# Kernel tuning notes

Hardware: AMD Instinct MI355X
Metric: run time of the kernel (lower is better)

Reference implementation:

```python
import jax, jax.numpy as jnp
import numpy as np
from jax import lax

N = 32768      # total nodes (8 graphs x 4096)
E = 262144     # edges (avg degree 8)
B = 8          # graphs in batch
TW = 25        # time window
H = 128        # hidden features
L = 6          # GNN layers
NV = 1         # n_variables (pos_t only)
SD = 1         # spatial dim
TMAX, TMIN, RES_T = 4.0, 0.0, 250.0
BD_LOW, BD_UP = 0.0, 16.0
EPS = 1e-5


def swish(x):
    return x * jax.nn.sigmoid(x)


def setup_inputs() -> dict:
    key = jax.random.key(0)
    ks = jax.random.split(key, 32)
    s = 0.05
    u = jax.random.normal(ks[0], (N, TW), jnp.float32)
    pos_t = jax.random.uniform(ks[1], (N, 1), jnp.float32) * TMAX
    pos_x = jax.random.uniform(ks[2], (N, 1), jnp.float32) * BD_UP
    pos = jnp.concatenate([pos_t, pos_x], axis=-1)
    edge_index = jax.random.randint(ks[3], (2, E), 0, N, jnp.int64)
    batch = jnp.repeat(jnp.arange(B, dtype=jnp.int64), N // B)
    d_in = TW + SD + NV          # 27
    d_msg = 2 * H + TW + SD + NV  # 282
    d_upd = H + H + NV            # 257
    We1 = jax.random.normal(ks[4], (d_in, H), jnp.float32) * s
    be1 = jnp.zeros((H,), jnp.float32)
    We2 = jax.random.normal(ks[5], (H, H), jnp.float32) * s
    be2 = jnp.zeros((H,), jnp.float32)
    Wm1 = jax.random.normal(ks[6], (L, d_msg, H), jnp.float32) * s
    bm1 = jnp.zeros((L, H), jnp.float32)
    Wm2 = jax.random.normal(ks[7], (L, H, H), jnp.float32) * s
    bm2 = jnp.zeros((L, H), jnp.float32)
    Wu1 = jax.random.normal(ks[8], (L, d_upd, H), jnp.float32) * s
    bu1 = jnp.zeros((L, H), jnp.float32)
    Wu2 = jax.random.normal(ks[9], (L, H, H), jnp.float32) * s
    bu2 = jnp.zeros((L, H), jnp.float32)
    Wc1 = jax.random.normal(ks[10], (8, 1, 16), jnp.float32) * s  # OIH
    bc1 = jnp.zeros((8,), jnp.float32)
    Wc2 = jax.random.normal(ks[11], (1, 8, 14), jnp.float32) * s
    bc2 = jnp.zeros((1,), jnp.float32)
    return dict(u=u, pos=pos, edge_index=edge_index, batch=batch,
                We1=We1, be1=be1, We2=We2, be2=be2,
                Wm1=Wm1, bm1=bm1, Wm2=Wm2, bm2=bm2,
                Wu1=Wu1, bu1=bu1, Wu2=Wu2, bu2=bu2,
                Wc1=Wc1, bc1=bc1, Wc2=Wc2, bc2=bc2)


def _mpnn(u, pos, edge_index, batch, We1, be1, We2, be2,
          Wm1, bm1, Wm2, bm2, Wu1, bu1, Wu2, bu2, Wc1, bc1, Wc2, bc2):
    src = edge_index[0]   # j (source)
    tgt = edge_index[1]   # i (target)
    pos_t = pos[:, 0:1] / TMAX
    pos_x = (pos[:, 1:] - BD_LOW) / (BD_UP - BD_LOW)
    variables = pos_t  # eq_variables empty -> only normalized time

    node_input = jnp.concatenate([u, pos_x, variables], axis=-1)  # [N, 27]
    h = swish(node_input @ We1 + be1)
    h = swish(h @ We2 + be2)

    # in-degree for scatter-mean (empty targets -> 0 like PyG mean)
    cnt = jnp.zeros((N,), jnp.float32).at[tgt].add(1.0)
    cnt = jnp.maximum(cnt, 1.0)[:, None]
    # per-graph node counts for InstanceNorm
    gcnt = jax.ops.segment_sum(jnp.ones((N,), jnp.float32), batch, num_segments=B)[:, None]

    u_diff_e = u[tgt] - u[src]          # [E, TW]
    p_diff_e = pos_x[tgt] - pos_x[src]  # [E, SD]
    var_i_e = variables[tgt]            # [E, NV]

    for l in range(L):
        # message: gather -> MLP per edge
        m_in = jnp.concatenate([h[tgt], h[src], u_diff_e, p_diff_e, var_i_e], axis=-1)  # [E, 282]
        msg = swish(m_in @ Wm1[l] + bm1[l])
        msg = swish(msg @ Wm2[l] + bm2[l])
        # scatter-mean aggregate onto targets
        agg = jax.ops.segment_sum(msg, tgt, num_segments=N) / cnt  # [N, H]
        # node update MLP, residual (in_features == out_features)
        up = jnp.concatenate([h, agg, variables], axis=-1)  # [N, 257]
        up = swish(up @ Wu1[l] + bu1[l])
        up = swish(up @ Wu2[l] + bu2[l])
        h = h + up
        # InstanceNorm per graph (no affine), biased variance
        mean = jax.ops.segment_sum(h, batch, num_segments=B) / gcnt      # [B, H]
        sq = jax.ops.segment_sum(h * h, batch, num_segments=B) / gcnt    # [B, H]
        var = sq - mean * mean
        h = (h - mean[batch]) / jnp.sqrt(var[batch] + EPS)

    # output CNN: tw=25 branch
    hc = h[:, None, :]  # [N, 1, 128]
    dn = ('NCH', 'OIH', 'NCH')
    c = lax.conv_general_dilated(hc, Wc1, (3,), 'VALID', dimension_numbers=dn) + bc1[None, :, None]
    c = swish(c)
    c = lax.conv_general_dilated(c, Wc2, (1,), 'VALID', dimension_numbers=dn) + bc2[None, :, None]
    diff = c[:, 0, :]  # [N, 25]

    dt = (TMAX - TMIN) / RES_T
    dt_cum = jnp.arange(1, TW + 1, dtype=jnp.float32) * dt  # cumsum of ones*dt
    out = u[:, -1:] + dt_cum[None, :] * diff
    return out


def reference(u, pos, edge_index, batch, We1, be1, We2, be2,
              Wm1, bm1, Wm2, bm2, Wu1, bu1, Wu2, bu2, Wc1, bc1, Wc2, bc2):
    return _mpnn(u, pos, edge_index, batch, We1, be1, We2, be2,
                 Wm1, bm1, Wm2, bm2, Wu1, bu1, Wu2, bu2, Wc1, bc1, Wc2, bc2)
```

## Files before the change

### kernel.cpp

```cpp
#include <hip/hip_runtime.h>
#include <stdint.h>

#define N_NODES 32768
#define N_EDGES 262144
#define NB 8
#define TW 25

typedef __attribute__((ext_vector_type(8))) short short8;
typedef __attribute__((ext_vector_type(4))) float floatx4;

#if defined(__has_builtin)
#if __has_builtin(__builtin_amdgcn_cvt_pk_bf16_f32)
#define HAVE_CVT_PK_BF16 1
#endif
#endif

__device__ __forceinline__ float swishf(float x) {
    return x * __builtin_amdgcn_rcpf(1.0f + __expf(-x));
}

__device__ __forceinline__ unsigned short f2bf(float x) {
    union { float f; unsigned u; } v; v.f = x;
    unsigned r = v.u + 0x7FFFu + ((v.u >> 16) & 1u);
    return (unsigned short)(r >> 16);
}
__device__ __forceinline__ unsigned pkbf(float a, float b) {
#ifdef HAVE_CVT_PK_BF16
    typedef __attribute__((ext_vector_type(2))) __bf16 bf16x2;
    union { bf16x2 v; unsigned u; } cv;
    cv.v = __builtin_amdgcn_cvt_pk_bf16_f32(a, b);
    return cv.u;
#else
    return (unsigned)f2bf(a) | ((unsigned)f2bf(b) << 16);
#endif
}
__device__ __forceinline__ float bf2f(unsigned short b) {
    union { unsigned u; float f; } v; v.u = ((unsigned)b) << 16; return v.f;
}
__device__ __forceinline__ float bflo(unsigned w) {
    union { unsigned u; float f; } v; v.u = w << 16; return v.f;
}
__device__ __forceinline__ float bfhi(unsigned w) {
    union { unsigned u; float f; } v; v.u = w & 0xffff0000u; return v.f;
}

__global__ void init_kernel(const float* __restrict__ pos, const float* __restrict__ u,
                            float* __restrict__ posx, float* __restrict__ post,
                            unsigned short* __restrict__ feat) {
    int i = blockIdx.x * 256 + threadIdx.x;
    if (i < N_NODES) {
        float pt = pos[i * 2 + 0] * 0.25f;
        float px = pos[i * 2 + 1] * 0.0625f;
        post[i] = pt;
        posx[i] = px;
        unsigned short f[32];
        #pragma unroll
        for (int k = 0; k < 25; ++k) f[k] = f2bf(u[(size_t)i * 25 + k]);
        f[25] = f2bf(px);
        f[26] = f2bf(pt);
        #pragma unroll
        for (int k = 27; k < 32; ++k) f[k] = 0;
        #pragma unroll
        for (int j = 0; j < 4; ++j)
            *(uint4*)(feat + (size_t)i * 32 + j * 8) = *(uint4*)&f[j * 8];
    }
}

__global__ void deg_kernel(const int* __restrict__ tgt, int* __restrict__ deg) {
    int i = blockIdx.x * 256 + threadIdx.x;
    if (i < N_EDGES) atomicAdd(&deg[tgt[i]], 1);
}

__global__ __launch_bounds__(1024) void scan_kernel(const int* __restrict__ deg,
                                                    int* __restrict__ cursor) {
    __shared__ int ps[1024];
    int t = threadIdx.x;
    int base = t * 32;
    int tot = 0;
    for (int i = 0; i < 32; ++i) tot += deg[base + i];
    ps[t] = tot;
    __syncthreads();
    for (int off = 1; off < 1024; off <<= 1) {
        int v = (t >= off) ? ps[t - off] : 0;
        __syncthreads();
        ps[t] += v;
        __syncthreads();
    }
    int run = ps[t] - tot;
    for (int i = 0; i < 32; ++i) {
        cursor[base + i] = run;
        run += deg[base + i];
    }
}

__global__ void scatter_kernel(const int* __restrict__ src, const int* __restrict__ tgt,
                               int* __restrict__ cursor,
                               int* __restrict__ src_s, int* __restrict__ tgt_s) {
    int i = blockIdx.x * 256 + threadIdx.x;
    if (i < N_EDGES) {
        int tg = tgt[i];
        int p = atomicAdd(&cursor[tg], 1);
        src_s[p] = src[i];
        tgt_s[p] = tg;
    }
}

__global__ __launch_bounds__(256) void pack_kernel(const float* __restrict__ W,
                                                   unsigned short* __restrict__ Wp,
                                                   int Kreal, int Kc, int total) {
    int id = blockIdx.x * 256 + threadIdx.x;
    if (id >= total) return;
    int lane = id & 63;
    int t8 = (id >> 6) & 7;
    int rest = id >> 9;
    int c = rest % Kc;
    int l = rest / Kc;
    int n = t8 * 16 + (lane & 15);
    int kb = c * 32 + (lane >> 4) * 8;
    short8 v;
    #pragma unroll
    for (int j = 0; j < 8; ++j) {
        int k = kb + j;
        float x = (k < Kreal) ? W[((size_t)l * Kreal + k) * 128 + n] : 0.f;
        v[j] = (short)f2bf(x);
    }
    *(short8*)(Wp + (size_t)id * 8) = v;
}

__global__ __launch_bounds__(256) void pack_cat_kernel(const float* __restrict__ Wm1,
                                                       const float* __restrict__ Wu1,
                                                       unsigned short* __restrict__ Wp) {
    int id = blockIdx.x * 256 + threadIdx.x;
    if (id >= 46080) return;
    int lane = id & 63;
    int tmp = id >> 6;
    int tile = tmp % 24;
    int tmp2 = tmp / 24;
    int c = tmp2 % 5;
    int l = tmp2 / 5;
    int n = tile * 16 + (lane & 15);
    int grp = n >> 7;
    int col = n & 127;
    int kb = c * 32 + (lane >> 4) * 8;
    const float* Wm = Wm1 + (size_t)l * 283 * 128;
    const float* Wu = Wu1 + (size_t)l * 257 * 128;
    short8 v;
    #pragma unroll
    for (int j = 0; j < 8; ++j) {
        int k = kb + j;
        float x = 0.f;
        if (grp == 2) {
            if (k < 128) x = Wu[(size_t)k * 128 + col];
        } else if (k < 128) {
            x = Wm[(size_t)(grp ? 128 + k : k) * 128 + col];
        } else if (k < 155) {
            int row = 256 + (k - 128);
            x = Wm[(size_t)row * 128 + col];
            if (grp) x = (row == 282) ? 0.f : -x;
        }
        v[j] = (short)f2bf(x);
    }
    *(short8*)(Wp + (size_t)id * 8) = v;
}

__global__ __launch_bounds__(256) void pack_upd_kernel(const float* __restrict__ Wu1,
                                                       unsigned short* __restrict__ Wp) {
    int id = blockIdx.x * 256 + threadIdx.x;
    if (id >= 15360) return;
    int lane = id & 63;
    int t8 = (id >> 6) & 7;
    int rest = id >> 9;
    int c = rest % 5;
    int l = rest / 5;
    int n = t8 * 16 + (lane & 15);
    int kb = c * 32 + (lane >> 4) * 8;
    const float* Wu = Wu1 + (size_t)l * 257 * 128;
    short8 v;
    #pragma unroll
    for (int j = 0; j < 8; ++j) {
        int k = kb + j;
        float x = 0.f;
        if (k < 128) x = Wu[(size_t)(128 + k) * 128 + n];
        else if (k == 128) x = Wu[(size_t)256 * 128 + n];
        v[j] = (short)f2bf(x);
    }
    *(short8*)(Wp + (size_t)id * 8) = v;
}

__global__ __launch_bounds__(256) void encoder_kernel(
    const float* __restrict__ u, const float* __restrict__ posx,
    const float* __restrict__ post,
    const float* __restrict__ We1, const float* __restrict__ be1,
    const float* __restrict__ We2, const float* __restrict__ be2,
    unsigned short* __restrict__ hraw, float* __restrict__ agg)
{
    __shared__ __align__(16) float As_[64 * 36];
    __shared__ __align__(16) float Ws[32 * 128];
    __shared__ __align__(16) float Ms[64 * 128];

    int t = threadIdx.x;
    int n0 = blockIdx.x * 64;
    int rg = t >> 5, cg = t & 31;

    {
        int r = t & 63, cseg = t >> 6;
        float4 z = make_float4(0.f, 0.f, 0.f, 0.f);
        #pragma unroll
        for (int j = 0; j < 8; ++j)
            *(float4*)(agg + (size_t)(n0 + r) * 128 + cseg * 32 + j * 4) = z;
    }

    float acc[8][4] = {};
    {
        int kk = t >> 3, cb = (t & 7) * 16;
        #pragma unroll
        for (int j = 0; j < 4; ++j) {
            float4 w = make_float4(0.f, 0.f, 0.f, 0.f);
            if (kk < 27) w = *(const float4*)&We1[kk * 128 + cb + j * 4];
            *(float4*)&Ws[kk * 128 + cb + j * 4] = w;
        }
        int el = t >> 2, kb = (t & 3) * 8, n = n0 + el;
        float v[8];
        #pragma unroll
        for (int j = 0; j < 8; ++j) {
            int k = kb + j;
            float x = 0.f;
            if (k < 25) x = u[n * 25 + k];
            else if (k == 25) x = posx[n];
            else if (k == 26) x = post[n];
            v[j] = x;
        }
        #pragma unroll
        for (int j = 0; j < 8; j += 4)
            *(float4*)&As_[el * 36 + kb + j] = make_float4(v[j], v[j+1], v[j+2], v[j+3]);
        __syncthreads();
        #pragma unroll 4
        for (int kk2 = 0; kk2 < 32; ++kk2) {
            float4 b = *(const float4*)&Ws[kk2 * 128 + cg * 4];
            float a[8];
            #pragma unroll
            for (int i = 0; i < 8; ++i) a[i] = As_[(rg * 8 + i) * 36 + kk2];
            #pragma unroll
            for (int i = 0; i < 8; ++i) {
                acc[i][0] += a[i] * b.x; acc[i][1] += a[i] * b.y;
                acc[i][2] += a[i] * b.z; acc[i][3] += a[i] * b.w;
            }
        }
        __syncthreads();
    }
    {
        float4 b1 = *(const float4*)&be1[cg * 4];
        #pragma unroll
        for (int i = 0; i < 8; ++i) {
            float4 m;
            m.x = swishf(acc[i][0] + b1.x);
            m.y = swishf(acc[i][1] + b1.y);
            m.z = swishf(acc[i][2] + b1.z);
            m.w = swishf(acc[i][3] + b1.w);
            *(float4*)&Ms[(rg * 8 + i) * 128 + cg * 4] = m;
        }
        __syncthreads();
    }
    float acc2[8][4] = {};
    for (int k0 = 0; k0 < 128; k0 += 32) {
        int kk = t >> 3, cb = (t & 7) * 16;
        #pragma unroll
        for (int j = 0; j < 4; ++j)
            *(float4*)&Ws[kk * 128 + cb + j * 4] =
                *(const float4*)&We2[(k0 + kk) * 128 + cb + j * 4];
        __syncthreads();
        #pragma unroll 4
        for (int kk2 = 0; kk2 < 32; ++kk2) {
            float4 b = *(const float4*)&Ws[kk2 * 128 + cg * 4];
            float a[8];
            #pragma unroll
            for (int i = 0; i < 8; ++i) a[i] = Ms[(rg * 8 + i) * 128 + (k0 + kk2)];
            #pragma unroll
            for (int i = 0; i < 8; ++i) {
                acc2[i][0] += a[i] * b.x; acc2[i][1] += a[i] * b.y;
                acc2[i][2] += a[i] * b.z; acc2[i][3] += a[i] * b.w;
            }
        }
        __syncthreads();
    }
    {
        float4 b2 = *(const float4*)&be2[cg * 4];
        #pragma unroll
        for (int i = 0; i < 8; ++i) {
            int n = n0 + rg * 8 + i;
            float4 o;
            o.x = swishf(acc2[i][0] + b2.x);
            o.y = swishf(acc2[i][1] + b2.y);
            o.z = swishf(acc2[i][2] + b2.z);
            o.w = swishf(acc2[i][3] + b2.w);
            uint2 pk;
            pk.x = pkbf(o.x, o.y);
            pk.y = pkbf(o.z, o.w);
            *(uint2*)(hraw + (size_t)n * 128 + cg * 4) = pk;
        }
    }
}

__global__ __launch_bounds__(512, 4) void premsg_kernel(
    const unsigned short* __restrict__ hraw,
    const float* __restrict__ stats_prev, int donorm,
    const unsigned short* __restrict__ feat,
    const unsigned short* __restrict__ Wp,
    const float* __restrict__ b1, const float* __restrict__ bu1,
    unsigned short* __restrict__ At, unsigned short* __restrict__ As,
    unsigned short* __restrict__ Uh)
{
    __shared__ __align__(16) unsigned short A[64 * 168];
    __shared__ float mean_s[128];
    __shared__ float rstd_s[128];

    int t = threadIdx.x;
    int n0 = blockIdx.x * 64;
    int bidx = n0 >> 12;

    if (t < 128) {
        float mn = 0.f, rs = 1.f;
        if (donorm) {
            float s1 = stats_prev[bidx * 128 + t] * (1.f / 4096.f);
            float s2 = stats_prev[(NB + bidx) * 128 + t] * (1.f / 4096.f);
            mn = s1;
            rs = rsqrtf(s2 - s1 * s1 + 1e-5f);
        }
        mean_s[t] = mn;
        rstd_s[t] = rs;
    }
    __syncthreads();

    {
        int r = t & 63, cseg = t >> 6;
        int n = n0 + r;
        uint4 raw0 = *(const uint4*)(hraw + (size_t)n * 128 + cseg * 16);
        uint4 raw1 = *(const uint4*)(hraw + (size_t)n * 128 + cseg * 16 + 8);
        unsigned pk[8];
        #pragma unroll
        for (int j = 0; j < 8; ++j) {
            unsigned word = (j < 4) ? ((const unsigned*)&raw0)[j]
                                    : ((const unsigned*)&raw1)[j - 4];
            int c0 = cseg * 16 + j * 2;
            float v0 = (bf2f((unsigned short)(word & 0xffffu)) - mean_s[c0]) * rstd_s[c0];
            float v1 = (bf2f((unsigned short)(word >> 16)) - mean_s[c0 + 1]) * rstd_s[c0 + 1];
            pk[j] = pkbf(v0, v1);
        }
        *(uint4*)(A + r * 168 + cseg * 16)     = *(uint4*)&pk[0];
        *(uint4*)(A + r * 168 + cseg * 16 + 8) = *(uint4*)&pk[4];
        if (cseg < 2) {
            uint4 f0 = *(const uint4*)(feat + (size_t)n * 32 + cseg * 16);
            uint4 f1 = *(const uint4*)(feat + (size_t)n * 32 + cseg * 16 + 8);
            *(uint4*)(A + r * 168 + 128 + cseg * 16)     = f0;
            *(uint4*)(A + r * 168 + 128 + cseg * 16 + 8) = f1;
        }
    }
    __syncthreads();

    int w = t >> 6, lane = t & 63, q = lane >> 4, m = lane & 15;
    floatx4 accT[4] = {};
    floatx4 accS[4] = {};
    floatx4 accU[4] = {};
    #pragma unroll
    for (int c = 0; c < 5; ++c) {
        short8 bT = *(const short8*)(Wp + ((size_t)(c * 24 + w) * 64 + lane) * 8);
        short8 bS = *(const short8*)(Wp + ((size_t)(c * 24 + 8 + w) * 64 + lane) * 8);
        short8 bU = *(const short8*)(Wp + ((size_t)(c * 24 + 16 + w) * 64 + lane) * 8);
        #pragma unroll
        for (int g2 = 0; g2 < 4; ++g2) {
            short8 a = *(const short8*)(A + (g2 * 16 + m) * 168 + c * 32 + q * 8);
            accT[g2] = __builtin_amdgcn_mfma_f32_16x16x32_bf16(a, bT, accT[g2], 0, 0, 0);
            accS[g2] = __builtin_amdgcn_mfma_f32_16x16x32_bf16(a, bS, accS[g2], 0, 0, 0);
            accU[g2] = __builtin_amdgcn_mfma_f32_16x16x32_bf16(a, bU, accU[g2], 0, 0, 0);
        }
    }
    int col = w * 16 + m;
    float bvT = b1[col];
    float bvU = bu1[col];
    #pragma unroll
    for (int g2 = 0; g2 < 4; ++g2) {
        #pragma unroll
        for (int r = 0; r < 4; ++r) {
            int row = g2 * 16 + q * 4 + r;
            size_t idx = (size_t)(n0 + row) * 128 + col;
            At[idx] = f2bf(accT[g2][r] + bvT);
            As[idx] = f2bf(accS[g2][r]);
        }
    }
    {
        unsigned up[8];
        #pragma unroll
        for (int g2 = 0; g2 < 4; ++g2) {
            up[g2 * 2]     = pkbf(accU[g2][0] + bvU, accU[g2][1] + bvU);
            up[g2 * 2 + 1] = pkbf(accU[g2][2] + bvU, accU[g2][3] + bvU);
        }
        unsigned short* dst = Uh + (size_t)blockIdx.x * 8192 + t * 16;
        *(uint4*)dst       = *(uint4*)&up[0];
        *(uint4*)(dst + 8) = *(uint4*)&up[4];
    }
}

__global__ __launch_bounds__(256, 8) void message_kernel(
    const unsigned short* __restrict__ At, const unsigned short* __restrict__ As,
    const int* __restrict__ src_s, const int* __restrict__ tgt_s,
    const unsigned short* __restrict__ W2p, const float* __restrict__ b2,
    float* __restrict__ agg, float* __restrict__ stats_cur)
{
    __shared__ __align__(16) unsigned short Cs[64 * 132];
    __shared__ int tgtS[64];

    int t = threadIdx.x;
    int e0 = blockIdx.x * 64;
    if (blockIdx.x == 0) {
        float4 z = make_float4(0.f, 0.f, 0.f, 0.f);
        *(float4*)&stats_cur[t * 8] = z;
        *(float4*)&stats_cur[t * 8 + 4] = z;
    }
    if (t < 64) tgtS[t] = tgt_s[e0 + t];
    __syncthreads();

    int w = t >> 6, lane = t & 63, q = lane >> 4, m = lane & 15;
    int erow = w * 16 + m;
    int e = e0 + erow;
    int gg = tgtS[erow];
    int ss = src_s[e];

    const unsigned short* atp = At + (size_t)gg * 128 + q * 8;
    const unsigned short* asp = As + (size_t)ss * 128 + q * 8;
    uint4 wa[4], wb[4];
    #pragma unroll
    for (int c = 0; c < 4; ++c) {
        wa[c] = *(const uint4*)(atp + c * 32);
        wb[c] = *(const uint4*)(asp + c * 32);
    }
    short8 af[4];
    #pragma unroll
    for (int c = 0; c < 4; ++c) {
        const unsigned* ua = (const unsigned*)&wa[c];
        const unsigned* ub = (const unsigned*)&wb[c];
        union { unsigned u[4]; short8 s; } pk_;
        #pragma unroll
        for (int j = 0; j < 4; ++j) {
            float lo = swishf(bflo(ua[j]) + bflo(ub[j]));
            float hi = swishf(bfhi(ua[j]) + bfhi(ub[j]));
            pk_.u[j] = pkbf(lo, hi);
        }
        af[c] = pk_.s;
    }

    floatx4 acc[8] = {};
    #pragma unroll
    for (int c = 0; c < 4; ++c) {
        #pragma unroll
        for (int t8 = 0; t8 < 8; ++t8) {
            short8 b = *(const short8*)(W2p + ((size_t)(c * 8 + t8) * 64 + lane) * 8);
            acc[t8] = __builtin_amdgcn_mfma_f32_16x16x32_bf16(af[c], b, acc[t8], 0, 0, 0);
        }
    }

    #pragma unroll
    for (int t8 = 0; t8 < 8; ++t8) {
        float bv = b2[t8 * 16 + m];
        unsigned p01 = pkbf(swishf(acc[t8][0] + bv), swishf(acc[t8][1] + bv));
        unsigned p23 = pkbf(swishf(acc[t8][2] + bv), swishf(acc[t8][3] + bv));
        int rb = (w * 16 + q * 4) * 132 + t8 * 16 + m;
        Cs[rb]           = (unsigned short)p01;
        Cs[rb + 132]     = (unsigned short)(p01 >> 16);
        Cs[rb + 2 * 132] = (unsigned short)p23;
        Cs[rb + 3 * 132] = (unsigned short)(p23 >> 16);
    }

    {
        int r0 = w * 16;
        int col0 = lane;
        float run0 = 0.f, run1 = 0.f;
        int prev = tgtS[r0];
        bool atStart = true;
        #pragma unroll 4
        for (int i = 0; i < 16; ++i) {
            int tg = tgtS[r0 + i];
            if (tg != prev) {
                float* d0 = &agg[(size_t)prev * 128 + col0];
                if (atStart) { atomicAdd(d0, run0); atomicAdd(d0 + 64, run1); }
                else         { d0[0] = run0;        d0[64] = run1; }
                run0 = 0.f; run1 = 0.f; prev = tg; atStart = false;
            }
            run0 += bf2f(Cs[(r0 + i) * 132 + col0]);
            run1 += bf2f(Cs[(r0 + i) * 132 + col0 + 64]);
        }
        float* d0 = &agg[(size_t)prev * 128 + col0];
        atomicAdd(d0, run0);
        atomicAdd(d0 + 64, run1);
    }
}

__global__ __launch_bounds__(512, 8) void update_kernel(
    unsigned short* __restrict__ hraw,
    const unsigned short* __restrict__ Uh,
    float* __restrict__ agg, const int* __restrict__ deg,
    const float* __restrict__ post,
    const float* __restrict__ stats_prev, int donorm,
    const unsigned short* __restrict__ W1p,
    const unsigned short* __restrict__ W2p, const float* __restrict__ b2,
    float* __restrict__ stats_cur)
{
    __shared__ __align__(16) unsigned short A[64 * 168];
    __shared__ __align__(16) unsigned short Msh[64 * 136];

    int t = threadIdx.x;
    int n0 = blockIdx.x * 64;
    int bidx = n0 >> 12;

    const unsigned short* usrc = Uh + (size_t)blockIdx.x * 8192 + t * 16;
    uint4 uh0 = *(const uint4*)usrc;
    uint4 uh1 = *(const uint4*)(usrc + 8);

    {
        int r = t & 63, cseg = t >> 6;
        int n = n0 + r;
        float ic = __builtin_amdgcn_rcpf(fmaxf((float)deg[n], 1.0f));
        const float* ap = agg + (size_t)n * 128 + cseg * 16;
        float4 v0 = *(const float4*)ap;
        float4 v1 = *(const float4*)(ap + 4);
        float4 v2 = *(const float4*)(ap + 8);
        float4 v3 = *(const float4*)(ap + 12);
        unsigned pa[8];
        pa[0] = pkbf(v0.x * ic, v0.y * ic);
        pa[1] = pkbf(v0.z * ic, v0.w * ic);
        pa[2] = pkbf(v1.x * ic, v1.y * ic);
        pa[3] = pkbf(v1.z * ic, v1.w * ic);
        pa[4] = pkbf(v2.x * ic, v2.y * ic);
        pa[5] = pkbf(v2.z * ic, v2.w * ic);
        pa[6] = pkbf(v3.x * ic, v3.y * ic);
        pa[7] = pkbf(v3.z * ic, v3.w * ic);
        *(uint4*)(A + r * 168 + cseg * 16)     = *(uint4*)&pa[0];
        *(uint4*)(A + r * 168 + cseg * 16 + 8) = *(uint4*)&pa[4];
        if (cseg < 4) {
            short8 z;
            #pragma unroll
            for (int k = 0; k < 8; ++k) z[k] = 0;
            if (cseg == 0) z[0] = (short)f2bf(post[n]);
            *(short8*)(A + r * 168 + 128 + cseg * 8) = z;
        }
    }
    __syncthreads();

    int w = t >> 6, lane = t & 63, q = lane >> 4, m = lane & 15;
    int col = w * 16 + m;

    floatx4 acc[4] = {};
    #pragma unroll
    for (int c = 0; c < 5; ++c) {
        short8 b = *(const short8*)(W1p + ((size_t)(c * 8 + w) * 64 + lane) * 8);
        #pragma unroll
        for (int g2 = 0; g2 < 4; ++g2) {
            short8 a = *(const short8*)(A + (g2 * 16 + m) * 168 + c * 32 + q * 8);
            acc[g2] = __builtin_amdgcn_mfma_f32_16x16x32_bf16(a, b, acc[g2], 0, 0, 0);
        }
    }
    {
        const unsigned* uu0 = (const unsigned*)&uh0;
        const unsigned* uu1 = (const unsigned*)&uh1;
        #pragma unroll
        for (int g2 = 0; g2 < 4; ++g2) {
            unsigned wlo = (g2 < 2) ? uu0[g2 * 2]     : uu1[(g2 - 2) * 2];
            unsigned whi = (g2 < 2) ? uu0[g2 * 2 + 1] : uu1[(g2 - 2) * 2 + 1];
            int rowb = g2 * 16 + q * 4;
            float v0 = swishf(acc[g2][0] + bflo(wlo));
            float v1 = swishf(acc[g2][1] + bfhi(wlo));
            float v2 = swishf(acc[g2][2] + bflo(whi));
            float v3 = swishf(acc[g2][3] + bfhi(whi));
            unsigned p01 = pkbf(v0, v1);
            unsigned p23 = pkbf(v2, v3);
            Msh[(rowb + 0) * 136 + col] = (unsigned short)p01;
            Msh[(rowb + 1) * 136 + col] = (unsigned short)(p01 >> 16);
            Msh[(rowb + 2) * 136 + col] = (unsigned short)p23;
            Msh[(rowb + 3) * 136 + col] = (unsigned short)(p23 >> 16);
        }
    }
    __syncthreads();

    floatx4 acc2[4] = {};
    #pragma unroll
    for (int c = 0; c < 4; ++c) {
        short8 b = *(const short8*)(W2p + ((size_t)(c * 8 + w) * 64 + lane) * 8);
        #pragma unroll
        for (int g2 = 0; g2 < 4; ++g2) {
            short8 a = *(const short8*)(Msh + (g2 * 16 + m) * 136 + c * 32 + q * 8);
            acc2[g2] = __builtin_amdgcn_mfma_f32_16x16x32_bf16(a, b, acc2[g2], 0, 0, 0);
        }
    }

    float mn = 0.f, rs = 1.f;
    if (donorm) {
        float s1 = stats_prev[bidx * 128 + col] * (1.f / 4096.f);
        float s2p = stats_prev[(NB + bidx) * 128 + col] * (1.f / 4096.f);
        mn = s1;
        rs = rsqrtf(s2p - s1 * s1 + 1e-5f);
    }
    float bv = b2[col];
    float s = 0.f, s2 = 0.f;
    #pragma unroll
    for (int g2 = 0; g2 < 4; ++g2) {
        #pragma unroll
        for (int r = 0; r < 4; ++r) {
            int row = g2 * 16 + q * 4 + r;
            size_t idx = (size_t)(n0 + row) * 128 + col;
            float res = (bf2f(hraw[idx]) - mn) * rs;
            float hv = res + swishf(acc2[g2][r] + bv);
            hraw[idx] = f2bf(hv);
            s += hv; s2 += hv * hv;
        }
    }
    s  += __shfl_xor(s, 16);  s  += __shfl_xor(s, 32);
    s2 += __shfl_xor(s2, 16); s2 += __shfl_xor(s2, 32);
    if (q == 0) {
        atomicAdd(&stats_cur[bidx * 128 + col], s);
        atomicAdd(&stats_cur[(NB + bidx) * 128 + col], s2);
    }
    {
        int r = t & 63, cseg = t >> 6;
        float4 z = make_float4(0.f, 0.f, 0.f, 0.f);
        #pragma unroll
        for (int j = 0; j < 4; ++j)
            *(float4*)(agg + (size_t)(n0 + r) * 128 + cseg * 16 + j * 4) = z;
    }
}

__global__ __launch_bounds__(256) void conv_kernel(
    const unsigned short* __restrict__ hraw, const float* __restrict__ stats,
    const float* __restrict__ u,
    const float* __restrict__ Wc1, const float* __restrict__ bc1,
    const float* __restrict__ Wc2, const float* __restrict__ bc2,
    float* __restrict__ out)
{
    __shared__ float hs[4][128];
    __shared__ float c1[4][8 * 40];
    int w = threadIdx.x >> 6, lane = threadIdx.x & 63;
    int n = blockIdx.x * 4 + w;
    int b = n >> 12;
    #pragma unroll
    for (int h2 = 0; h2 < 2; ++h2) {
        int c = lane + h2 * 64;
        float s1 = stats[b * 128 + c] * (1.f / 4096.f);
        float s2 = stats[(NB + b) * 128 + c] * (1.f / 4096.f);
        float rs = rsqrtf(s2 - s1 * s1 + 1e-5f);
        hs[w][c] = (bf2f(hraw[(size_t)n * 128 + c]) - s1) * rs;
    }
    __syncthreads();
    for (int idx = lane; idx < 304; idx += 64) {
        int o = idx / 38, p = idx % 38;
        float s = bc1[o];
        #pragma unroll
        for (int k = 0; k < 16; ++k) s += hs[w][p * 3 + k] * Wc1[o * 16 + k];
        c1[w][o * 40 + p] = swishf(s);
    }
    __syncthreads();
    if (lane < TW) {
        float s = bc2[0];
        #pragma unroll
        for (int o = 0; o < 8; ++o)
            for (int k = 0; k < 14; ++k)
                s += c1[w][o * 40 + lane + k] * Wc2[o * 14 + k];
        float dt_cum = (float)(lane + 1) * (4.0f / 250.0f);
        out[n * TW + lane] = u[n * 25 + 24] + dt_cum * s;
    }
}

extern "C" void kernel_launch(void* const* d_in, const int* in_sizes, int n_in,
                              void* d_out, int out_size, void* d_ws, size_t ws_size,
                              hipStream_t stream)
{
    const float* u   = (const float*)d_in[0];
    const float* pos = (const float*)d_in[1];
    const int*   ei  = (const int*)d_in[2];
    const float* We1 = (const float*)d_in[4];
    const float* be1 = (const float*)d_in[5];
    const float* We2 = (const float*)d_in[6];
    const float* be2 = (const float*)d_in[7];
    const float* Wm1 = (const float*)d_in[8];
    const float* bm1 = (const float*)d_in[9];
    const float* Wm2 = (const float*)d_in[10];
    const float* bm2 = (const float*)d_in[11];
    const float* Wu1 = (const float*)d_in[12];
    const float* bu1 = (const float*)d_in[13];
    const float* Wu2 = (const float*)d_in[14];
    const float* bu2 = (const float*)d_in[15];
    const float* Wc1 = (const float*)d_in[16];
    const float* bc1 = (const float*)d_in[17];
    const float* Wc2 = (const float*)d_in[18];
    const float* bc2 = (const float*)d_in[19];
    float* out = (float*)d_out;

    char* base = (char*)d_ws;
    size_t off = 0;
    auto alloc = [&](size_t bytes) -> char* {
        char* r = base + off;
        off = (off + bytes + 511) & ~(size_t)511;
        return r;
    };
    unsigned short* hraw   = (unsigned short*)alloc((size_t)N_NODES * 128 * 2);
    float*          agg    = (float*)alloc((size_t)N_NODES * 128 * 4);
    unsigned short* At     = (unsigned short*)alloc((size_t)N_NODES * 128 * 2);
    unsigned short* As     = (unsigned short*)alloc((size_t)N_NODES * 128 * 2);
    unsigned short* Uh     = (unsigned short*)alloc((size_t)N_NODES * 128 * 2);
    float*          posx   = (float*)alloc(N_NODES * 4);
    float*          post   = (float*)alloc(N_NODES * 4);
    unsigned short* feat   = (unsigned short*)alloc((size_t)N_NODES * 32 * 2);
    float*          statsA = (float*)alloc(2 * NB * 128 * 4);
    float*          statsB = (float*)alloc(2 * NB * 128 * 4);
    int*            deg    = (int*)alloc(N_NODES * 4);
    int*            cursor = (int*)alloc(N_NODES * 4);
    int*            src_s  = (int*)alloc((size_t)N_EDGES * 4);
    int*            tgt_s  = (int*)alloc((size_t)N_EDGES * 4);
    unsigned short* Wcat1p = (unsigned short*)alloc((size_t)46080 * 8 * 2);
    unsigned short* Wm2p   = (unsigned short*)alloc((size_t)6 * 4 * 4096 * 2);
    unsigned short* Wu1p   = (unsigned short*)alloc((size_t)15360 * 8 * 2);
    unsigned short* Wu2p   = (unsigned short*)alloc((size_t)6 * 4 * 4096 * 2);
    (void)ws_size;

    const int* srcp = ei;
    const int* tgtp = ei + N_EDGES;

    init_kernel<<<N_NODES / 256, 256, 0, stream>>>(pos, u, posx, post, feat);
    hipMemsetAsync(deg, 0, N_NODES * sizeof(int), stream);
    deg_kernel<<<N_EDGES / 256, 256, 0, stream>>>(tgtp, deg);
    scan_kernel<<<1, 1024, 0, stream>>>(deg, cursor);
    scatter_kernel<<<N_EDGES / 256, 256, 0, stream>>>(srcp, tgtp, cursor, src_s, tgt_s);
    encoder_kernel<<<N_NODES / 64, 256, 0, stream>>>(u, posx, post, We1, be1, We2, be2,
                                                     hraw, agg);
    {
        pack_cat_kernel<<<180, 256, 0, stream>>>(Wm1, Wu1, Wcat1p);
        pack_upd_kernel<<<60, 256, 0, stream>>>(Wu1, Wu1p);
        int tot2 = 6 * 4 * 512;
        pack_kernel<<<(tot2 + 255) / 256, 256, 0, stream>>>(Wm2, Wm2p, 128, 4, tot2);
        pack_kernel<<<(tot2 + 255) / 256, 256, 0, stream>>>(Wu2, Wu2p, 128, 4, tot2);
    }

    for (int l = 0; l < 6; ++l) {
        float* stats_cur  = (l & 1) ? statsB : statsA;
        float* stats_prev = (l & 1) ? statsA : statsB;
        int donorm = (l > 0) ? 1 : 0;
        premsg_kernel<<<N_NODES / 64, 512, 0, stream>>>(
            hraw, stats_prev, donorm, feat,
            Wcat1p + (size_t)l * 5 * 24 * 512, bm1 + l * 128, bu1 + l * 128,
            At, As, Uh);
        message_kernel<<<N_EDGES / 64, 256, 0, stream>>>(
            At, As, src_s, tgt_s,
            Wm2p + (size_t)l * 4 * 4096, bm2 + l * 128, agg, stats_cur);
        update_kernel<<<N_NODES / 64, 512, 0, stream>>>(
            hraw, Uh, agg, deg, post, stats_prev, donorm,
            Wu1p + (size_t)l * 5 * 8 * 512,
            Wu2p + (size_t)l * 4 * 4096, bu2 + l * 128, stats_cur);
    }

    conv_kernel<<<N_NODES / 4, 256, 0, stream>>>(hraw, statsB, u, Wc1, bc1, Wc2, bc2, out);
}
```

Baseline: 644.8 us.

## Process two edge tiles per message block with software-prefetched gathers

Each message_kernel block now handles 128 edges in two 64-edge passes instead of one. The gathers for the second tile's source and target rows are issued during the first tile's MFMA and scatter phases, so global load latency overlaps with compute. The grid is halved and the occupancy hint drops from 8 to 6 waves per SIMD. That gives fewer resident waves and higher register pressure in exchange for the software-prefetched gathers.

```diff
diff --git a/kernel.cpp b/kernel.cpp
--- a/kernel.cpp
+++ b/kernel.cpp
@@ -400,44 +400,48 @@
     }
 }
 
-__global__ __launch_bounds__(256, 8) void message_kernel(
+__global__ __launch_bounds__(256, 6) void message_kernel(
     const unsigned short* __restrict__ At, const unsigned short* __restrict__ As,
     const int* __restrict__ src_s, const int* __restrict__ tgt_s,
     const unsigned short* __restrict__ W2p, const float* __restrict__ b2,
     float* __restrict__ agg, float* __restrict__ stats_cur)
 {
     __shared__ __align__(16) unsigned short Cs[64 * 132];
-    __shared__ int tgtS[64];
+    __shared__ int tgtS[128];
 
     int t = threadIdx.x;
-    int e0 = blockIdx.x * 64;
+    int e0 = blockIdx.x * 128;
     if (blockIdx.x == 0) {
         float4 z = make_float4(0.f, 0.f, 0.f, 0.f);
         *(float4*)&stats_cur[t * 8] = z;
         *(float4*)&stats_cur[t * 8 + 4] = z;
     }
-    if (t < 64) tgtS[t] = tgt_s[e0 + t];
+    if (t < 128) tgtS[t] = tgt_s[e0 + t];
     __syncthreads();
 
     int w = t >> 6, lane = t & 63, q = lane >> 4, m = lane & 15;
     int erow = w * 16 + m;
-    int e = e0 + erow;
-    int gg = tgtS[erow];
-    int ss = src_s[e];
-
-    const unsigned short* atp = At + (size_t)gg * 128 + q * 8;
-    const unsigned short* asp = As + (size_t)ss * 128 + q * 8;
-    uint4 wa[4], wb[4];
+
+    int gg0 = tgtS[erow];
+    int ss0 = src_s[e0 + erow];
+    const unsigned short* atp0 = At + (size_t)gg0 * 128 + q * 8;
+    const unsigned short* asp0 = As + (size_t)ss0 * 128 + q * 8;
+    uint4 wa0[4], wb0[4];
     #pragma unroll
     for (int c = 0; c < 4; ++c) {
-        wa[c] = *(const uint4*)(atp + c * 32);
-        wb[c] = *(const uint4*)(asp + c * 32);
-    }
+        wa0[c] = *(const uint4*)(atp0 + c * 32);
+        wb0[c] = *(const uint4*)(asp0 + c * 32);
+    }
+    int gg1 = tgtS[64 + erow];
+    int ss1 = src_s[e0 + 64 + erow];
+    const unsigned short* atp1 = At + (size_t)gg1 * 128 + q * 8;
+    const unsigned short* asp1 = As + (size_t)ss1 * 128 + q * 8;
+
     short8 af[4];
     #pragma unroll
     for (int c = 0; c < 4; ++c) {
-        const unsigned* ua = (const unsigned*)&wa[c];
-        const unsigned* ub = (const unsigned*)&wb[c];
+        const unsigned* ua = (const unsigned*)&wa0[c];
+        const unsigned* ub = (const unsigned*)&wb0[c];
         union { unsigned u[4]; short8 s; } pk_;
         #pragma unroll
         for (int j = 0; j < 4; ++j) {
@@ -448,27 +452,36 @@
         af[c] = pk_.s;
     }
 
-    floatx4 acc[8] = {};
-    #pragma unroll
-    for (int c = 0; c < 4; ++c) {
+    uint4 wb1[4];
+    #pragma unroll
+    for (int c = 0; c < 4; ++c) wb1[c] = *(const uint4*)(asp1 + c * 32);
+
+    {
+        floatx4 acc[8] = {};
+        #pragma unroll
+        for (int c = 0; c < 4; ++c) {
+            #pragma unroll
+            for (int t8 = 0; t8 < 8; ++t8) {
+                short8 b = *(const short8*)(W2p + ((size_t)(c * 8 + t8) * 64 + lane) * 8);
+                acc[t8] = __builtin_amdgcn_mfma_f32_16x16x32_bf16(af[c], b, acc[t8], 0, 0, 0);
+            }
+        }
         #pragma unroll
         for (int t8 = 0; t8 < 8; ++t8) {
-            short8 b = *(const short8*)(W2p + ((size_t)(c * 8 + t8) * 64 + lane) * 8);
-            acc[t8] = __builtin_amdgcn_mfma_f32_16x16x32_bf16(af[c], b, acc[t8], 0, 0, 0);
-        }
-    }
-
-    #pragma unroll
-    for (int t8 = 0; t8 < 8; ++t8) {
-        float bv = b2[t8 * 16 + m];
-        unsigned p01 = pkbf(swishf(acc[t8][0] + bv), swishf(acc[t8][1] + bv));
-        unsigned p23 = pkbf(swishf(acc[t8][2] + bv), swishf(acc[t8][3] + bv));
-        int rb = (w * 16 + q * 4) * 132 + t8 * 16 + m;
-        Cs[rb]           = (unsigned short)p01;
-        Cs[rb + 132]     = (unsigned short)(p01 >> 16);
-        Cs[rb + 2 * 132] = (unsigned short)p23;
-        Cs[rb + 3 * 132] = (unsigned short)(p23 >> 16);
-    }
+            float bv = b2[t8 * 16 + m];
+            unsigned p01 = pkbf(swishf(acc[t8][0] + bv), swishf(acc[t8][1] + bv));
+            unsigned p23 = pkbf(swishf(acc[t8][2] + bv), swishf(acc[t8][3] + bv));
+            int rb = (w * 16 + q * 4) * 132 + t8 * 16 + m;
+            Cs[rb]           = (unsigned short)p01;
+            Cs[rb + 132]     = (unsigned short)(p01 >> 16);
+            Cs[rb + 2 * 132] = (unsigned short)p23;
+            Cs[rb + 3 * 132] = (unsigned short)(p23 >> 16);
+        }
+    }
+
+    uint4 wa1[4];
+    #pragma unroll
+    for (int c = 0; c < 4; ++c) wa1[c] = *(const uint4*)(atp1 + c * 32);
 
     {
         int r0 = w * 16;
@@ -479,6 +492,66 @@
         #pragma unroll 4
         for (int i = 0; i < 16; ++i) {
             int tg = tgtS[r0 + i];
+            if (tg != prev) {
+                float* d0 = &agg[(size_t)prev * 128 + col0];
+                if (atStart) { atomicAdd(d0, run0); atomicAdd(d0 + 64, run1); }
+                else         { d0[0] = run0;        d0[64] = run1; }
+                run0 = 0.f; run1 = 0.f; prev = tg; atStart = false;
+            }
+            run0 += bf2f(Cs[(r0 + i) * 132 + col0]);
+            run1 += bf2f(Cs[(r0 + i) * 132 + col0 + 64]);
+        }
+        float* d0 = &agg[(size_t)prev * 128 + col0];
+        atomicAdd(d0, run0);
+        atomicAdd(d0 + 64, run1);
+    }
+
+    #pragma unroll
+    for (int c = 0; c < 4; ++c) {
+        const unsigned* ua = (const unsigned*)&wa1[c];
+        const unsigned* ub = (const unsigned*)&wb1[c];
+        union { unsigned u[4]; short8 s; } pk_;
+        #pragma unroll
+        for (int j = 0; j < 4; ++j) {
+            float lo = swishf(bflo(ua[j]) + bflo(ub[j]));
+            float hi = swishf(bfhi(ua[j]) + bfhi(ub[j]));
+            pk_.u[j] = pkbf(lo, hi);
+        }
+        af[c] = pk_.s;
+    }
+
+    {
+        floatx4 acc[8] = {};
+        #pragma unroll
+        for (int c = 0; c < 4; ++c) {
+            #pragma unroll
+            for (int t8 = 0; t8 < 8; ++t8) {
+                short8 b = *(const short8*)(W2p + ((size_t)(c * 8 + t8) * 64 + lane) * 8);
+                acc[t8] = __builtin_amdgcn_mfma_f32_16x16x32_bf16(af[c], b, acc[t8], 0, 0, 0);
+            }
+        }
+        #pragma unroll
+        for (int t8 = 0; t8 < 8; ++t8) {
+            float bv = b2[t8 * 16 + m];
+            unsigned p01 = pkbf(swishf(acc[t8][0] + bv), swishf(acc[t8][1] + bv));
+            unsigned p23 = pkbf(swishf(acc[t8][2] + bv), swishf(acc[t8][3] + bv));
+            int rb = (w * 16 + q * 4) * 132 + t8 * 16 + m;
+            Cs[rb]           = (unsigned short)p01;
+            Cs[rb + 132]     = (unsigned short)(p01 >> 16);
+            Cs[rb + 2 * 132] = (unsigned short)p23;
+            Cs[rb + 3 * 132] = (unsigned short)(p23 >> 16);
+        }
+    }
+
+    {
+        int r0 = w * 16;
+        int col0 = lane;
+        float run0 = 0.f, run1 = 0.f;
+        int prev = tgtS[64 + r0];
+        bool atStart = true;
+        #pragma unroll 4
+        for (int i = 0; i < 16; ++i) {
+            int tg = tgtS[64 + r0 + i];
             if (tg != prev) {
                 float* d0 = &agg[(size_t)prev * 128 + col0];
                 if (atStart) { atomicAdd(d0, run0); atomicAdd(d0 + 64, run1); }
@@ -745,7 +818,7 @@
             hraw, stats_prev, donorm, feat,
             Wcat1p + (size_t)l * 5 * 24 * 512, bm1 + l * 128, bu1 + l * 128,
             At, As, Uh);
-        message_kernel<<<N_EDGES / 64, 256, 0, stream>>>(
+        message_kernel<<<N_EDGES / 128, 256, 0, stream>>>(
             At, As, src_s, tgt_s,
             Wm2p + (size_t)l * 4 * 4096, bm2 + l * 128, agg, stats_cur);
         update_kernel<<<N_NODES / 64, 512, 0, stream>>>(
```

After: 775.7 us. 20.3% more time.
